# Kernel optimization log

Measured on AMD Instinct MI355X. Metric: run time of the kernel, lower is better.

Reference implementation:

```python
import jax, jax.numpy as jnp
import numpy as np

B, T, D, H = 4, 2048, 768, 12
DH = D // H  # 64
SCALE = float(DH) ** 0.5  # NOTE: original code MULTIPLIES by sqrt(d_head)


def setup_inputs() -> dict:
    key = jax.random.key(0)
    k1, k2, k3 = jax.random.split(key, 3)
    x = jax.random.normal(k1, (B, T, D), dtype=jnp.float32)
    w_qkv = jax.random.normal(k2, (3 * D, D), dtype=jnp.float32) * (D ** -0.5)
    w_out = jax.random.normal(k3, (D, D), dtype=jnp.float32) * (D ** -0.5)
    return {"x": x, "w_qkv": w_qkv, "w_out": w_out}


def reference(x, w_qkv, w_out):
    b, t, d = x.shape
    # qkv_layer: Linear(d, 3d, bias=False) -> x @ W.T
    qkv = jnp.einsum('btd,ed->bte', x, w_qkv)  # [b, t, 3d]
    # rearrange 'b t (d k h) -> k b h t d' with k=3, h=H: split as (DH, 3, H)
    qkv = qkv.reshape(b, t, DH, 3, H)
    qkv = jnp.transpose(qkv, (3, 0, 4, 1, 2))  # [3, b, h, t, dh]
    q, k, v = qkv[0], qkv[1], qkv[2]
    # energy multiplied (faithfully) by sqrt(d_head)
    energy = jnp.einsum('bhid,bhjd->bhij', q, k) * SCALE
    attn = jax.nn.softmax(energy, axis=-1)
    o = jnp.einsum('bhij,bhjd->bhid', attn, v)  # [b, h, t, dh]
    # rearrange 'b h t d -> b t (h d)'
    o = jnp.transpose(o, (0, 2, 1, 3)).reshape(b, t, d)
    return jnp.einsum('btd,ed->bte', o, w_out)
```

## Files before the change

kernel.cpp:

```cpp
#include <hip/hip_runtime.h>
#include <hip/hip_bf16.h>
#include <cstdint>
#include <cstddef>

#define Bsz 4
#define Tsz 2048
#define Dsz 768
#define Hsz 12
#define DHsz 64
#define Msz (Bsz * Tsz)
#define K2 1536
#define K3 2304
#define QSCALE 11.5415603f

typedef __attribute__((ext_vector_type(8))) short short8;
typedef __attribute__((ext_vector_type(4))) float floatx4;

#if __has_builtin(__builtin_amdgcn_exp2f)
#define EXP2(x) __builtin_amdgcn_exp2f(x)
#else
#define EXP2(x) exp2f(x)
#endif

typedef const __attribute__((address_space(1))) unsigned int* gas1;
typedef __attribute__((address_space(3))) unsigned int* las3;
__device__ __forceinline__ void dma16(const unsigned short* g, unsigned short* l) {
  __builtin_amdgcn_global_load_lds((gas1)g, (las3)l, 16, 0, 0);
}

__device__ __forceinline__ unsigned short f2bf(float f) {
  union { float f; unsigned u; } v; v.f = f;
  unsigned u = v.u;
  unsigned r = u + 0x7fffu + ((u >> 16) & 1u);
  return (unsigned short)(r >> 16);
}
__device__ __forceinline__ float bf2f(unsigned short h) {
  union { unsigned u; float f; } v; v.u = ((unsigned)h) << 16; return v.f;
}
__device__ __forceinline__ unsigned pk_bf2(float a, float b) {
  union { __hip_bfloat162 b2; unsigned u; } cv;
  cv.b2 = __float22bfloat162_rn(make_float2(a, b));
  return cv.u;
}

#define TREAD(arr, row, s) \
  (*reinterpret_cast<const short8*>(&(arr)[((row) << 6) + ((((s) * 4 + quad) ^ ((row) & 7)) << 3)]))

__global__ void split_x(const float* __restrict__ src,
                        unsigned short* __restrict__ dst) {
  int i = (blockIdx.x * blockDim.x + threadIdx.x) * 4;
  int row = i / Dsz, col = i % Dsz;
  float4 v = *reinterpret_cast<const float4*>(src + i);
  ushort4 h, l;
  h.x = f2bf(v.x); l.x = f2bf(v.x - bf2f(h.x));
  h.y = f2bf(v.y); l.y = f2bf(v.y - bf2f(h.y));
  h.z = f2bf(v.z); l.z = f2bf(v.z - bf2f(h.z));
  h.w = f2bf(v.w); l.w = f2bf(v.w - bf2f(h.w));
  unsigned short* base = dst + (size_t)row * K2 + col;
  *reinterpret_cast<ushort4*>(base) = h;
  *reinterpret_cast<ushort4*>(base + Dsz) = l;
}

__global__ void split_w(const float* __restrict__ src,
                        unsigned short* __restrict__ dst) {
  int i = (blockIdx.x * blockDim.x + threadIdx.x) * 4;
  int rp = i / Dsz, c = i % Dsz;
  int kk = rp / Dsz;
  int rem = rp - kk * Dsz;
  int h = rem >> 6, d = rem & 63;
  const float* s = src + (size_t)(d * 36 + kk * 12 + h) * Dsz + c;
  float4 v = *reinterpret_cast<const float4*>(s);
  ushort4 hh, ll;
  hh.x = f2bf(v.x); ll.x = f2bf(v.x - bf2f(hh.x));
  hh.y = f2bf(v.y); ll.y = f2bf(v.y - bf2f(hh.y));
  hh.z = f2bf(v.z); ll.z = f2bf(v.z - bf2f(hh.z));
  hh.w = f2bf(v.w); ll.w = f2bf(v.w - bf2f(hh.w));
  unsigned short* base = dst + (size_t)rp * K2 + c;
  *reinterpret_cast<ushort4*>(base) = hh;
  *reinterpret_cast<ushort4*>(base + Dsz) = ll;
}

__global__ void cvt_f32_bf16(const float* __restrict__ src,
                             unsigned short* __restrict__ dst, int n) {
  int i = (blockIdx.x * blockDim.x + threadIdx.x) * 4;
  int stride = gridDim.x * blockDim.x * 4;
  for (; i < n; i += stride) {
    float4 v = *reinterpret_cast<const float4*>(src + i);
    ushort4 o;
    o.x = f2bf(v.x); o.y = f2bf(v.y); o.z = f2bf(v.z); o.w = f2bf(v.w);
    *reinterpret_cast<ushort4*>(dst + i) = o;
  }
}

__launch_bounds__(256, 3)
__global__ void gemm_qkv(const unsigned short* __restrict__ xs,
                         const unsigned short* __restrict__ wsb,
                         unsigned short* __restrict__ Qhp,
                         unsigned short* __restrict__ Qlp,
                         unsigned short* __restrict__ Khp,
                         unsigned short* __restrict__ Klp,
                         unsigned short* __restrict__ Vtp) {
  __shared__ unsigned short As[128 * 64], Bs[128 * 64];
  const int mt128 = blockIdx.x;
  const int nblk = blockIdx.y;
  const int tid = threadIdx.x;
  const int w = tid >> 6, lane = tid & 63, l16 = lane & 15, quad = lane >> 4;
  const int lrow = lane >> 3;
  const int lgl  = (lane & 7) ^ lrow;

  floatx4 acc[2][8];
#pragma unroll
  for (int mt = 0; mt < 2; ++mt)
#pragma unroll
    for (int nt = 0; nt < 8; ++nt) acc[mt][nt] = (floatx4){0.f, 0.f, 0.f, 0.f};

  const size_t abase = (size_t)(mt128 * 128) * K2;
  const size_t bbase = (size_t)(nblk * 128) * K2;

  for (int kc = 0; kc < K3; kc += 64) {
    const int akc = (kc < 768)  ? kc : kc - 768;
    const int bkc = (kc < 1536) ? kc : kc - 1536;
    __syncthreads();
#pragma unroll
    for (int j = 0; j < 4; ++j) {
      const int R0 = w * 32 + j * 8;
      dma16(xs + abase + (size_t)(R0 + lrow) * K2 + akc + lgl * 8, &As[R0 * 64]);
    }
#pragma unroll
    for (int j = 0; j < 4; ++j) {
      const int R0 = w * 32 + j * 8;
      dma16(wsb + bbase + (size_t)(R0 + lrow) * K2 + bkc + lgl * 8, &Bs[R0 * 64]);
    }
    __syncthreads();
#pragma unroll
    for (int s = 0; s < 2; ++s) {
      short8 a[2];
#pragma unroll
      for (int mt = 0; mt < 2; ++mt) a[mt] = TREAD(As, w * 32 + mt * 16 + l16, s);
#pragma unroll
      for (int nt = 0; nt < 8; ++nt) {
        short8 b = TREAD(Bs, nt * 16 + l16, s);
#pragma unroll
        for (int mt = 0; mt < 2; ++mt)
          acc[mt][nt] = __builtin_amdgcn_mfma_f32_16x16x32_bf16(a[mt], b, acc[mt][nt], 0, 0, 0);
      }
    }
  }
  const int kk = nblk / 6;
  const int h0 = (nblk % 6) * 2;
  unsigned short* dh_ = (kk == 0) ? Qhp : Khp;
  unsigned short* dl_ = (kk == 0) ? Qlp : Klp;
  const float sc = (kk == 0) ? QSCALE : 1.0f;
#pragma unroll
  for (int mt = 0; mt < 2; ++mt) {
    const int mbase = mt128 * 128 + w * 32 + mt * 16 + quad * 4;
    const int b = mbase >> 11;
    const int t0 = mbase & (Tsz - 1);
#pragma unroll
    for (int nt = 0; nt < 8; ++nt) {
      const int h = h0 + (nt >> 2);
      const int d = (nt & 3) * 16 + l16;
      const size_t hoff = (size_t)(b * Hsz + h) * Tsz * DHsz;
      if (kk == 2) {
        uint2 pk;
        pk.x = pk_bf2(acc[mt][nt][0], acc[mt][nt][1]);
        pk.y = pk_bf2(acc[mt][nt][2], acc[mt][nt][3]);
        *reinterpret_cast<uint2*>(&Vtp[hoff + (size_t)d * Tsz + t0]) = pk;
      } else {
#pragma unroll
        for (int r = 0; r < 4; ++r) {
          float v = acc[mt][nt][r] * sc;
          unsigned short hv = f2bf(v);
          dh_[hoff + (size_t)(t0 + r) * DHsz + d] = hv;
          dl_[hoff + (size_t)(t0 + r) * DHsz + d] = f2bf(v - bf2f(hv));
        }
      }
    }
  }
}

__launch_bounds__(256, 3)
__global__ void attn(const unsigned short* __restrict__ Qhp,
                     const unsigned short* __restrict__ Qlp,
                     const unsigned short* __restrict__ Khp,
                     const unsigned short* __restrict__ Klp,
                     const unsigned short* __restrict__ Vtp,
                     unsigned short* __restrict__ Ob) {
  __shared__ unsigned short Ksh[64 * 64], Ksl[64 * 64], Vs[64 * 64];
  __shared__ unsigned short plT[4][2][16][68];
  const int bid = blockIdx.x;
  const int xcd = bid & 7, slot = bid >> 3;
  const int bh = xcd * 6 + (slot >> 4);
  const int qt = slot & 15;
  const int tid = threadIdx.x;
  const int w = tid >> 6, lane = tid & 63, l16 = lane & 15, quad = lane >> 4;
  const int lrow = lane >> 3;
  const int lgl  = (lane & 7) ^ lrow;
  const size_t hoff = (size_t)bh * Tsz * DHsz;
  const unsigned short* Kh = Khp + hoff;
  const unsigned short* Kl = Klp + hoff;
  const unsigned short* Vt = Vtp + hoff;

  short8 qh[2][2], ql[2][2];
#pragma unroll
  for (int mt = 0; mt < 2; ++mt) {
    const size_t qoff = hoff + (size_t)(qt * 128 + w * 32 + mt * 16 + l16) * DHsz + quad * 8;
    qh[mt][0] = *reinterpret_cast<const short8*>(Qhp + qoff);
    qh[mt][1] = *reinterpret_cast<const short8*>(Qhp + qoff + 32);
    ql[mt][0] = *reinterpret_cast<const short8*>(Qlp + qoff);
    ql[mt][1] = *reinterpret_cast<const short8*>(Qlp + qoff + 32);
  }

  floatx4 Of[2][4];
#pragma unroll
  for (int mt = 0; mt < 2; ++mt)
#pragma unroll
    for (int nt = 0; nt < 4; ++nt) Of[mt][nt] = (floatx4){0.f, 0.f, 0.f, 0.f};
  float m_i[2] = {-1e30f, -1e30f};
  float l_i[2] = {0.f, 0.f};

  for (int kt = 0; kt < Tsz; kt += 64) {
    __syncthreads();
#pragma unroll
    for (int j = 0; j < 2; ++j) {
      const int R0 = w * 16 + j * 8;
      dma16(Kh + (size_t)(kt + R0 + lrow) * DHsz + lgl * 8, &Ksh[R0 * 64]);
      dma16(Kl + (size_t)(kt + R0 + lrow) * DHsz + lgl * 8, &Ksl[R0 * 64]);
      dma16(Vt + (size_t)(R0 + lrow) * Tsz + kt + lgl * 8,  &Vs[R0 * 64]);
    }
    __syncthreads();

    floatx4 S[2][4];
#pragma unroll
    for (int mt = 0; mt < 2; ++mt)
#pragma unroll
      for (int nt = 0; nt < 4; ++nt) S[mt][nt] = (floatx4){0.f, 0.f, 0.f, 0.f};
#pragma unroll
    for (int s = 0; s < 2; ++s) {
#pragma unroll
      for (int nt = 0; nt < 4; ++nt) {
        short8 kf_h = TREAD(Ksh, nt * 16 + l16, s);
        short8 kf_l = TREAD(Ksl, nt * 16 + l16, s);
        S[0][nt] = __builtin_amdgcn_mfma_f32_16x16x32_bf16(kf_h, qh[0][s], S[0][nt], 0, 0, 0);
        S[0][nt] = __builtin_amdgcn_mfma_f32_16x16x32_bf16(kf_l, qh[0][s], S[0][nt], 0, 0, 0);
        S[0][nt] = __builtin_amdgcn_mfma_f32_16x16x32_bf16(kf_h, ql[0][s], S[0][nt], 0, 0, 0);
        S[1][nt] = __builtin_amdgcn_mfma_f32_16x16x32_bf16(kf_h, qh[1][s], S[1][nt], 0, 0, 0);
        S[1][nt] = __builtin_amdgcn_mfma_f32_16x16x32_bf16(kf_l, qh[1][s], S[1][nt], 0, 0, 0);
        S[1][nt] = __builtin_amdgcn_mfma_f32_16x16x32_bf16(kf_h, ql[1][s], S[1][nt], 0, 0, 0);
      }
    }

#pragma unroll
    for (int mt = 0; mt < 2; ++mt) {
      float mx = -1e30f;
#pragma unroll
      for (int nt = 0; nt < 4; ++nt)
#pragma unroll
        for (int r = 0; r < 4; ++r) mx = fmaxf(mx, S[mt][nt][r]);
      mx = fmaxf(mx, __shfl_xor(mx, 16));
      mx = fmaxf(mx, __shfl_xor(mx, 32));
      float mnew = fmaxf(m_i[mt], mx);
      float alpha = EXP2(m_i[mt] - mnew);
      m_i[mt] = mnew;
      float ls = 0.f;
#pragma unroll
      for (int nt = 0; nt < 4; ++nt) {
        float p0 = EXP2(S[mt][nt][0] - mnew);
        float p1 = EXP2(S[mt][nt][1] - mnew);
        float p2 = EXP2(S[mt][nt][2] - mnew);
        float p3 = EXP2(S[mt][nt][3] - mnew);
        ls += (p0 + p1) + (p2 + p3);
        uint2 pk;
        pk.x = pk_bf2(p0, p1);
        pk.y = pk_bf2(p2, p3);
        *reinterpret_cast<uint2*>(&plT[w][mt][l16][nt * 16 + quad * 4]) = pk;
      }
      l_i[mt] = l_i[mt] * alpha + ls;
#pragma unroll
      for (int nt = 0; nt < 4; ++nt) {
        Of[mt][nt][0] *= alpha; Of[mt][nt][1] *= alpha;
        Of[mt][nt][2] *= alpha; Of[mt][nt][3] *= alpha;
      }
    }

    short8 pf[2][2];
#pragma unroll
    for (int s = 0; s < 2; ++s) {
      pf[0][s] = *reinterpret_cast<const short8*>(&plT[w][0][l16][s * 32 + quad * 8]);
      pf[1][s] = *reinterpret_cast<const short8*>(&plT[w][1][l16][s * 32 + quad * 8]);
    }
#pragma unroll
    for (int nt = 0; nt < 4; ++nt) {
#pragma unroll
      for (int s = 0; s < 2; ++s) {
        short8 vf = TREAD(Vs, nt * 16 + l16, s);
        Of[0][nt] = __builtin_amdgcn_mfma_f32_16x16x32_bf16(vf, pf[0][s], Of[0][nt], 0, 0, 0);
        Of[1][nt] = __builtin_amdgcn_mfma_f32_16x16x32_bf16(vf, pf[1][s], Of[1][nt], 0, 0, 0);
      }
    }
  }

  const int b = bh / Hsz, h = bh % Hsz;
#pragma unroll
  for (int mt = 0; mt < 2; ++mt) {
    float ls = l_i[mt];
    ls += __shfl_xor(ls, 16);
    ls += __shfl_xor(ls, 32);
    float inv = 1.0f / ls;
    int t = qt * 128 + w * 32 + mt * 16 + l16;
    unsigned short* orow = Ob + (size_t)(b * Tsz + t) * Dsz + h * DHsz;
#pragma unroll
    for (int nt = 0; nt < 4; ++nt) {
      uint2 pk;
      pk.x = pk_bf2(Of[mt][nt][0] * inv, Of[mt][nt][1] * inv);
      pk.y = pk_bf2(Of[mt][nt][2] * inv, Of[mt][nt][3] * inv);
      *reinterpret_cast<uint2*>(&orow[nt * 16 + quad * 4]) = pk;
    }
  }
}

__launch_bounds__(256, 3)
__global__ void gemm_out(const unsigned short* __restrict__ ob,
                         const unsigned short* __restrict__ wb,
                         float* __restrict__ out) {
  __shared__ unsigned short As[128 * 64];
  __shared__ unsigned short Bs[128 * 64];
  const int mt128 = blockIdx.x;
  const int n0 = blockIdx.y * 128;
  const int tid = threadIdx.x;
  const int w = tid >> 6, lane = tid & 63, l16 = lane & 15, quad = lane >> 4;
  const int lrow = lane >> 3;
  const int lgl  = (lane & 7) ^ lrow;

  floatx4 acc[2][8];
#pragma unroll
  for (int mt = 0; mt < 2; ++mt)
#pragma unroll
    for (int nt = 0; nt < 8; ++nt) acc[mt][nt] = (floatx4){0.f, 0.f, 0.f, 0.f};

  const size_t abase = (size_t)(mt128 * 128) * Dsz;
  const size_t bbase = (size_t)n0 * Dsz;

  for (int kc = 0; kc < Dsz; kc += 64) {
    __syncthreads();
#pragma unroll
    for (int j = 0; j < 4; ++j) {
      const int R0 = w * 32 + j * 8;
      dma16(ob + abase + (size_t)(R0 + lrow) * Dsz + kc + lgl * 8, &As[R0 * 64]);
    }
#pragma unroll
    for (int j = 0; j < 4; ++j) {
      const int R0 = w * 32 + j * 8;
      dma16(wb + bbase + (size_t)(R0 + lrow) * Dsz + kc + lgl * 8, &Bs[R0 * 64]);
    }
    __syncthreads();
#pragma unroll
    for (int s = 0; s < 2; ++s) {
      short8 a[2];
#pragma unroll
      for (int mt = 0; mt < 2; ++mt) a[mt] = TREAD(As, w * 32 + mt * 16 + l16, s);
#pragma unroll
      for (int nt = 0; nt < 8; ++nt) {
        short8 b = TREAD(Bs, nt * 16 + l16, s);
#pragma unroll
        for (int mt = 0; mt < 2; ++mt)
          acc[mt][nt] = __builtin_amdgcn_mfma_f32_16x16x32_bf16(a[mt], b, acc[mt][nt], 0, 0, 0);
      }
    }
  }
#pragma unroll
  for (int mt = 0; mt < 2; ++mt) {
    const int mbase = mt128 * 128 + w * 32 + mt * 16 + quad * 4;
#pragma unroll
    for (int nt = 0; nt < 8; ++nt) {
      int n = n0 + nt * 16 + l16;
#pragma unroll
      for (int r = 0; r < 4; ++r) {
        out[(size_t)(mbase + r) * Dsz + n] = acc[mt][nt][r];
      }
    }
  }
}

extern "C" void kernel_launch(void* const* d_in, const int* in_sizes, int n_in,
                              void* d_out, int out_size, void* d_ws, size_t ws_size,
                              hipStream_t stream) {
  const float* x     = (const float*)d_in[0];
  const float* w_qkv = (const float*)d_in[1];
  const float* w_out = (const float*)d_in[2];
  float* out = (float*)d_out;

  unsigned short* ws = (unsigned short*)d_ws;
  const size_t nXs = (size_t)Msz * K2;
  const size_t nWs = (size_t)3 * Dsz * K2;
  const size_t nWo = (size_t)Dsz * Dsz;
  const size_t nHd = (size_t)Bsz * Hsz * Tsz * DHsz;

  unsigned short* xs  = ws;
  unsigned short* wsb = xs + nXs;
  unsigned short* wob = wsb + nWs;
  unsigned short* Qhp = wob + nWo;
  unsigned short* Qlp = Qhp + nHd;
  unsigned short* Khp = Qlp + nHd;
  unsigned short* Klp = Khp + nHd;
  unsigned short* Vtp = Klp + nHd;
  unsigned short* Ob  = xs;

  split_x<<<(int)(nXs / 2 / 1024), 256, 0, stream>>>(x, xs);
  split_w<<<(int)(nWs / 2 / 1024), 256, 0, stream>>>(w_qkv, wsb);
  cvt_f32_bf16<<<256, 256, 0, stream>>>(w_out, wob, (int)nWo);
  gemm_qkv<<<dim3(64, 18), 256, 0, stream>>>(xs, wsb, Qhp, Qlp, Khp, Klp, Vtp);
  attn<<<768, 256, 0, stream>>>(Qhp, Qlp, Khp, Klp, Vtp, Ob);
  gemm_out<<<dim3(64, 6), 256, 0, stream>>>(Ob, wob, out);
}
```

Before: 327.7 us.

## Restructure QKV GEMM per head with split-bf16 terms and skip low terms for V

The QKV GEMM now computes one head (64 output columns) per block, with the hi/lo split-bf16 terms loaded into separate LDS buffers instead of being walked as one concatenated K=2304 loop. V blocks skip the low-part loads and MFMAs, which cuts work for a third of the outputs. Grid order is swapped so blocks sharing a weight tile launch adjacently, and gemm_out gets the same swap. In exchange, each block does fewer MFMAs per A-tile load and there are twice as many blocks.

```diff
diff --git a/kernel.cpp b/kernel.cpp
--- a/kernel.cpp
+++ b/kernel.cpp
@@ -10,7 +10,6 @@
 #define DHsz 64
 #define Msz (Bsz * Tsz)
 #define K2 1536
-#define K3 2304
 #define QSCALE 11.5415603f
 
 typedef __attribute__((ext_vector_type(8))) short short8;
@@ -100,79 +99,98 @@
                          unsigned short* __restrict__ Khp,
                          unsigned short* __restrict__ Klp,
                          unsigned short* __restrict__ Vtp) {
-  __shared__ unsigned short As[128 * 64], Bs[128 * 64];
-  const int mt128 = blockIdx.x;
-  const int nblk = blockIdx.y;
+  __shared__ unsigned short Ah[128 * 64], Al[128 * 64];
+  __shared__ unsigned short Bh[64 * 64],  Bl[64 * 64];
+  const int nblk = blockIdx.x;
+  const int mt128 = blockIdx.y;
+  const int kk = nblk / 12;
+  const int h  = nblk % 12;
   const int tid = threadIdx.x;
   const int w = tid >> 6, lane = tid & 63, l16 = lane & 15, quad = lane >> 4;
   const int lrow = lane >> 3;
   const int lgl  = (lane & 7) ^ lrow;
 
-  floatx4 acc[2][8];
+  floatx4 acc[2][4];
 #pragma unroll
   for (int mt = 0; mt < 2; ++mt)
 #pragma unroll
-    for (int nt = 0; nt < 8; ++nt) acc[mt][nt] = (floatx4){0.f, 0.f, 0.f, 0.f};
+    for (int nt = 0; nt < 4; ++nt) acc[mt][nt] = (floatx4){0.f, 0.f, 0.f, 0.f};
 
   const size_t abase = (size_t)(mt128 * 128) * K2;
-  const size_t bbase = (size_t)(nblk * 128) * K2;
-
-  for (int kc = 0; kc < K3; kc += 64) {
-    const int akc = (kc < 768)  ? kc : kc - 768;
-    const int bkc = (kc < 1536) ? kc : kc - 1536;
+  const size_t bbase = (size_t)(kk * Dsz + h * 64) * K2;
+
+  for (int kc = 0; kc < Dsz; kc += 64) {
     __syncthreads();
 #pragma unroll
     for (int j = 0; j < 4; ++j) {
       const int R0 = w * 32 + j * 8;
-      dma16(xs + abase + (size_t)(R0 + lrow) * K2 + akc + lgl * 8, &As[R0 * 64]);
-    }
-#pragma unroll
-    for (int j = 0; j < 4; ++j) {
-      const int R0 = w * 32 + j * 8;
-      dma16(wsb + bbase + (size_t)(R0 + lrow) * K2 + bkc + lgl * 8, &Bs[R0 * 64]);
+      const size_t g = abase + (size_t)(R0 + lrow) * K2 + kc + lgl * 8;
+      dma16(xs + g, &Ah[R0 * 64]);
+      if (kk != 2) dma16(xs + g + Dsz, &Al[R0 * 64]);
+    }
+#pragma unroll
+    for (int j = 0; j < 2; ++j) {
+      const int R0 = w * 16 + j * 8;
+      const size_t g = bbase + (size_t)(R0 + lrow) * K2 + kc + lgl * 8;
+      dma16(wsb + g, &Bh[R0 * 64]);
+      if (kk != 2) dma16(wsb + g + Dsz, &Bl[R0 * 64]);
     }
     __syncthreads();
 #pragma unroll
     for (int s = 0; s < 2; ++s) {
-      short8 a[2];
-#pragma unroll
-      for (int mt = 0; mt < 2; ++mt) a[mt] = TREAD(As, w * 32 + mt * 16 + l16, s);
-#pragma unroll
-      for (int nt = 0; nt < 8; ++nt) {
-        short8 b = TREAD(Bs, nt * 16 + l16, s);
+      short8 ah[2], al[2];
+#pragma unroll
+      for (int mt = 0; mt < 2; ++mt) ah[mt] = TREAD(Ah, w * 32 + mt * 16 + l16, s);
+      if (kk != 2) {
+#pragma unroll
+        for (int mt = 0; mt < 2; ++mt) al[mt] = TREAD(Al, w * 32 + mt * 16 + l16, s);
+      }
+#pragma unroll
+      for (int nt = 0; nt < 4; ++nt) {
+        short8 bh = TREAD(Bh, nt * 16 + l16, s);
 #pragma unroll
         for (int mt = 0; mt < 2; ++mt)
-          acc[mt][nt] = __builtin_amdgcn_mfma_f32_16x16x32_bf16(a[mt], b, acc[mt][nt], 0, 0, 0);
-      }
-    }
-  }
-  const int kk = nblk / 6;
-  const int h0 = (nblk % 6) * 2;
-  unsigned short* dh_ = (kk == 0) ? Qhp : Khp;
-  unsigned short* dl_ = (kk == 0) ? Qlp : Klp;
-  const float sc = (kk == 0) ? QSCALE : 1.0f;
+          acc[mt][nt] = __builtin_amdgcn_mfma_f32_16x16x32_bf16(ah[mt], bh, acc[mt][nt], 0, 0, 0);
+        if (kk != 2) {
+          short8 bl = TREAD(Bl, nt * 16 + l16, s);
+#pragma unroll
+          for (int mt = 0; mt < 2; ++mt) {
+            acc[mt][nt] = __builtin_amdgcn_mfma_f32_16x16x32_bf16(ah[mt], bl, acc[mt][nt], 0, 0, 0);
+            acc[mt][nt] = __builtin_amdgcn_mfma_f32_16x16x32_bf16(al[mt], bh, acc[mt][nt], 0, 0, 0);
+          }
+        }
+      }
+    }
+  }
 #pragma unroll
   for (int mt = 0; mt < 2; ++mt) {
     const int mbase = mt128 * 128 + w * 32 + mt * 16 + quad * 4;
     const int b = mbase >> 11;
+    const size_t hoff = (size_t)(b * Hsz + h) * Tsz * DHsz;
     const int t0 = mbase & (Tsz - 1);
-#pragma unroll
-    for (int nt = 0; nt < 8; ++nt) {
-      const int h = h0 + (nt >> 2);
-      const int d = (nt & 3) * 16 + l16;
-      const size_t hoff = (size_t)(b * Hsz + h) * Tsz * DHsz;
-      if (kk == 2) {
+    if (kk == 2) {
+      unsigned short* dst = Vtp + hoff;
+#pragma unroll
+      for (int nt = 0; nt < 4; ++nt) {
+        int d = nt * 16 + l16;
         uint2 pk;
         pk.x = pk_bf2(acc[mt][nt][0], acc[mt][nt][1]);
         pk.y = pk_bf2(acc[mt][nt][2], acc[mt][nt][3]);
-        *reinterpret_cast<uint2*>(&Vtp[hoff + (size_t)d * Tsz + t0]) = pk;
-      } else {
+        *reinterpret_cast<uint2*>(&dst[(size_t)d * Tsz + t0]) = pk;
+      }
+    } else {
+      const float sc = (kk == 0) ? QSCALE : 1.0f;
+      unsigned short* dh_ = ((kk == 0) ? Qhp : Khp) + hoff;
+      unsigned short* dl_ = ((kk == 0) ? Qlp : Klp) + hoff;
+#pragma unroll
+      for (int nt = 0; nt < 4; ++nt) {
+        int d = nt * 16 + l16;
 #pragma unroll
         for (int r = 0; r < 4; ++r) {
           float v = acc[mt][nt][r] * sc;
           unsigned short hv = f2bf(v);
-          dh_[hoff + (size_t)(t0 + r) * DHsz + d] = hv;
-          dl_[hoff + (size_t)(t0 + r) * DHsz + d] = f2bf(v - bf2f(hv));
+          dh_[(size_t)(t0 + r) * DHsz + d] = hv;
+          dl_[(size_t)(t0 + r) * DHsz + d] = f2bf(v - bf2f(hv));
         }
       }
     }
@@ -325,8 +343,8 @@
                          float* __restrict__ out) {
   __shared__ unsigned short As[128 * 64];
   __shared__ unsigned short Bs[128 * 64];
-  const int mt128 = blockIdx.x;
-  const int n0 = blockIdx.y * 128;
+  const int n0 = blockIdx.x * 128;
+  const int mt128 = blockIdx.y;
   const int tid = threadIdx.x;
   const int w = tid >> 6, lane = tid & 63, l16 = lane & 15, quad = lane >> 4;
   const int lrow = lane >> 3;
@@ -409,7 +427,7 @@
   split_x<<<(int)(nXs / 2 / 1024), 256, 0, stream>>>(x, xs);
   split_w<<<(int)(nWs / 2 / 1024), 256, 0, stream>>>(w_qkv, wsb);
   cvt_f32_bf16<<<256, 256, 0, stream>>>(w_out, wob, (int)nWo);
-  gemm_qkv<<<dim3(64, 18), 256, 0, stream>>>(xs, wsb, Qhp, Qlp, Khp, Klp, Vtp);
+  gemm_qkv<<<dim3(36, 64), 256, 0, stream>>>(xs, wsb, Qhp, Qlp, Khp, Klp, Vtp);
   attn<<<768, 256, 0, stream>>>(Qhp, Qlp, Khp, Klp, Vtp, Ob);
-  gemm_out<<<dim3(64, 6), 256, 0, stream>>>(Ob, wob, out);
-}
+  gemm_out<<<dim3(6, 64), 256, 0, stream>>>(Ob, wob, out);
+}
```

New measurement: 297.0 us. -9.4%, faster.
